# Kernel tuning notes

Measured on AMD Instinct MI355X. Metric: run time of the kernel, lower is better.

## Reference

```python
import jax, jax.numpy as jnp
import numpy as np

WS = 8  # window size
NH = 6  # num heads


def _rel_pos_index(ws):
    coords = jnp.stack(jnp.meshgrid(jnp.arange(ws), jnp.arange(ws), indexing='ij'))  # (2, ws, ws)
    cf = coords.reshape(2, -1)                      # (2, ws*ws)
    rel = cf[:, :, None] - cf[:, None, :]           # (2, ws2, ws2)
    return (rel[0] + ws - 1) * (2 * ws - 1) + (rel[1] + ws - 1)  # (ws2, ws2) int


def setup_inputs() -> dict:
    key = jax.random.key(0)
    k1, k2, k3, k4, k5 = jax.random.split(key, 5)
    B, H, W, C = 4, 256, 256, 192
    dim = C
    x = jax.random.normal(k1, (B, H * W, C), dtype=jnp.float32)
    qkv_w = jax.random.normal(k2, (3 * dim, dim), dtype=jnp.float32) * (dim ** -0.5)
    proj_w = jax.random.normal(k3, (dim, dim), dtype=jnp.float32) * (dim ** -0.5)
    proj_b = jax.random.normal(k4, (dim,), dtype=jnp.float32) * 0.01
    rpb_table = jax.random.normal(k5, ((2 * WS - 1) ** 2, NH), dtype=jnp.float32) * 0.02
    return {"x": x, "qkv_w": qkv_w, "proj_w": proj_w, "proj_b": proj_b,
            "rpb_table": rpb_table, "H": H, "W": W}


def reference(x, qkv_w, proj_w, proj_b, rpb_table, H, W):
    B, L, C = x.shape
    ws, nh = WS, NH
    hd = C // nh
    scale = hd ** -0.5
    ws2 = ws * ws

    pad_r = (ws - W % ws) % ws
    pad_b = (ws - H % ws) % ws
    Hp, Wp = H + pad_b, W + pad_r
    xi = x.reshape(B, H, W, C)
    if pad_r > 0 or pad_b > 0:
        xi = jnp.pad(xi, ((0, 0), (0, pad_b), (0, pad_r), (0, 0)))

    # window partition -> (nW, ws2, C)
    win = xi.reshape(B, Hp // ws, ws, Wp // ws, ws, C)
    win = win.transpose(0, 1, 3, 2, 4, 5).reshape(-1, ws2, C)

    # qkv projection (no bias)
    qkv = (win @ qkv_w.T).reshape(-1, ws2, 3, nh, hd)
    q = qkv[:, :, 0].transpose(0, 2, 1, 3) * scale  # (nW, nh, ws2, hd)
    k = qkv[:, :, 1].transpose(0, 2, 1, 3)
    v = qkv[:, :, 2].transpose(0, 2, 1, 3)

    attn = jnp.einsum('nhqd,nhkd->nhqk', q, k)      # (nW, nh, ws2, ws2)
    bias = rpb_table[_rel_pos_index(ws)]            # (ws2, ws2, nh)
    attn = attn + bias.transpose(2, 0, 1)[None]
    attn = jax.nn.softmax(attn, axis=-1)

    out = jnp.einsum('nhqk,nhkd->nhqd', attn, v)    # (nW, nh, ws2, hd)
    out = out.transpose(0, 2, 1, 3).reshape(-1, ws2, C)
    out = out @ proj_w.T + proj_b

    # window reverse
    xo = out.reshape(B, Hp // ws, Wp // ws, ws, ws, C)
    xo = xo.transpose(0, 1, 3, 2, 4, 5).reshape(B, Hp, Wp, C)
    if pad_r > 0 or pad_b > 0:
        xo = xo[:, :H, :W, :]
    return xo.reshape(B, H * W, C)
```

## Files before the change

kernel.cpp:

```cpp
#include <hip/hip_runtime.h>

typedef _Float16 f16;
typedef _Float16 f16x8 __attribute__((ext_vector_type(8)));
typedef _Float16 f16x4 __attribute__((ext_vector_type(4)));
typedef __fp16 h16x2 __attribute__((ext_vector_type(2)));
typedef float f32x4 __attribute__((ext_vector_type(4)));

constexpr int HDIM = 256, WDIM = 256, C_ = 192, NH_ = 6;
constexpr float SCALE = 0.17677669529663687f;
constexpr float L2E = 1.4426950408889634f;
constexpr float SCALE2 = SCALE * L2E;
constexpr int XP = 200;
constexpr int BUF = 64 * XP;

#define SCHED_FENCE() __builtin_amdgcn_sched_barrier(0)

constexpr size_t OFF_WQ   = 0;
constexpr size_t OFF_WP   = 221184;
constexpr size_t OFF_BIAS = 294912;

__global__ __launch_bounds__(256) void prep_kernel(const float* __restrict__ qkv_w,
                                                   const float* __restrict__ proj_w,
                                                   const float* __restrict__ rpb,
                                                   f16* __restrict__ wqp, f16* __restrict__ wpp,
                                                   float* __restrict__ biasp) {
    int i = blockIdx.x * 256 + threadIdx.x;
    if (i < 13824) {
        int lane = i & 63, rest = i >> 6;
        int ks = rest % 6; rest /= 6;
        int dt = rest & 1; rest >>= 1;
        int c = rest % 3, w = rest / 3;
        int l15 = lane & 15, lg = lane >> 4;
        int row = c * 192 + w * 32 + dt * 16 + l15;
        int col = ks * 32 + lg * 8;
        float sc = (c == 0) ? SCALE2 : 1.0f;
#pragma unroll
        for (int j = 0; j < 8; ++j) wqp[(size_t)i * 8 + j] = (f16)(qkv_w[row * 192 + col + j] * sc);
    } else if (i < 18432) {
        int g = i - 13824;
        int lane = g & 63, rest = g >> 6;
        int ks = rest % 6; rest /= 6;
        int nt = rest & 1, w = rest >> 1;
        int l15 = lane & 15, lg = lane >> 4;
        int row = w * 32 + nt * 16 + l15;
        int col = ks * 32 + lg * 8;
#pragma unroll
        for (int j = 0; j < 8; ++j) wpp[(size_t)g * 8 + j] = (f16)proj_w[row * 192 + col + j];
    } else if (i < 24576) {
        int g = i - 18432;
        int lane = g & 63;
        int kt = (g >> 6) & 3, qt = (g >> 8) & 3, h = g >> 10;
        int q = qt * 16 + (lane & 15);
#pragma unroll
        for (int j = 0; j < 4; ++j) {
            int k = kt * 16 + (lane >> 4) * 4 + j;
            int dy = (q >> 3) - (k >> 3) + 7;
            int dx = (q & 7) - (k & 7) + 7;
            biasp[(size_t)g * 4 + j] = rpb[(dy * 15 + dx) * NH_ + h] * L2E;
        }
    }
}

__global__ __launch_bounds__(256, 3) void fused_kernel(const float* __restrict__ x,
                                                       const f16* __restrict__ wqp,
                                                       const f16* __restrict__ wpp,
                                                       const float* __restrict__ pb,
                                                       const float* __restrict__ biasp,
                                                       float* __restrict__ out) {
    __shared__ f16 xlds[2 * BUF];
    const int tid = threadIdx.x;
    const int v = tid >> 6;
    const int lane = tid & 63;
    const int l15 = lane & 15, lg = lane >> 4;
    const int wb = blockIdx.x * 2;
    const int win = wb + (v >> 1);
    const int b = win >> 10, wy = (win >> 5) & 31, wx = win & 31;
    f16* mylds = xlds + (v >> 1) * BUF;

#pragma unroll
    for (int grp = 0; grp < 3; ++grp) {
#pragma unroll
        for (int it8 = 0; it8 < 8; ++it8) {
            int u = tid + (grp * 8 + it8) * 256;
            int wh = (u >= 3072) ? 1 : 0;
            int r = u - wh * 3072;
            int row = r / 48, c4 = r - row * 48;
            int ws = wb + wh;
            int bs = ws >> 10, wys = (ws >> 5) & 31, wxs = ws & 31;
            int gy = wys * 8 + (row >> 3), gx = wxs * 8 + (row & 7);
            float4 vv = *((const float4*)(x + ((size_t)((bs * HDIM + gy) * WDIM + gx)) * C_ + c4 * 4));
            h16x2 p0 = __builtin_amdgcn_cvt_pkrtz(vv.x, vv.y);
            h16x2 p1 = __builtin_amdgcn_cvt_pkrtz(vv.z, vv.w);
            f16x4 o4;
            o4[0] = (f16)p0[0]; o4[1] = (f16)p0[1]; o4[2] = (f16)p1[0]; o4[3] = (f16)p1[1];
            *((f16x4*)(xlds + wh * BUF + row * XP + c4 * 4)) = o4;
        }
        SCHED_FENCE();
    }
    __syncthreads();

    f16x4 oreg[3][4][2];

#pragma unroll
    for (int hh = 0; hh < 3; ++hh) {
        const int head = (v & 1) * 3 + hh;
        const f16x8* wqb   = (const f16x8*)wqp + (size_t)head * 36 * 64 + lane;
        const f32x4* bbase = (const f32x4*)biasp + (size_t)head * 16 * 64 + lane;
        SCHED_FENCE();

        f16x4 qf[2][4], kf[2][4];
        {
            f32x4 aq[2][4], ak[2][4];
#pragma unroll
            for (int ii = 0; ii < 4; ++ii)
#pragma unroll
                for (int jj = 0; jj < 2; ++jj) {
                    f32x4 z = {0.f, 0.f, 0.f, 0.f};
                    aq[jj][ii] = z; ak[jj][ii] = z;
                }
            __builtin_amdgcn_s_setprio(1);
#pragma unroll
            for (int ks = 0; ks < 6; ++ks) {
                f16x8 Wq0 = wqb[(size_t)(     ks) * 64], Wq1 = wqb[(size_t)( 6 + ks) * 64];
                f16x8 Wk0 = wqb[(size_t)(12 + ks) * 64], Wk1 = wqb[(size_t)(18 + ks) * 64];
#pragma unroll
                for (int tt = 0; tt < 4; ++tt) {
                    f16x8 xt = *((const f16x8*)(mylds + (tt * 16 + l15) * XP + ks * 32 + lg * 8));
                    aq[0][tt] = __builtin_amdgcn_mfma_f32_16x16x32_f16(Wq0, xt, aq[0][tt], 0, 0, 0);
                    aq[1][tt] = __builtin_amdgcn_mfma_f32_16x16x32_f16(Wq1, xt, aq[1][tt], 0, 0, 0);
                    ak[0][tt] = __builtin_amdgcn_mfma_f32_16x16x32_f16(Wk0, xt, ak[0][tt], 0, 0, 0);
                    ak[1][tt] = __builtin_amdgcn_mfma_f32_16x16x32_f16(Wk1, xt, ak[1][tt], 0, 0, 0);
                }
            }
            __builtin_amdgcn_s_setprio(0);
#pragma unroll
            for (int dt = 0; dt < 2; ++dt)
#pragma unroll
                for (int tt = 0; tt < 4; ++tt)
#pragma unroll
                    for (int ii = 0; ii < 4; ++ii) {
                        qf[dt][tt][ii] = (f16)(aq[dt][tt][ii]);
                        kf[dt][tt][ii] = (f16)(ak[dt][tt][ii]);
                    }
        }
        SCHED_FENCE();

        f16x4 vf[4][2];
        {
            f32x4 av[4][2];
#pragma unroll
            for (int ii = 0; ii < 4; ++ii)
#pragma unroll
                for (int jj = 0; jj < 2; ++jj) { f32x4 z = {0.f,0.f,0.f,0.f}; av[ii][jj] = z; }
            __builtin_amdgcn_s_setprio(1);
#pragma unroll
            for (int ks = 0; ks < 6; ++ks) {
                f16x8 W0 = wqb[(size_t)(24 + ks) * 64], W1 = wqb[(size_t)(30 + ks) * 64];
#pragma unroll
                for (int tt = 0; tt < 4; ++tt) {
                    f16x8 xt = *((const f16x8*)(mylds + (tt * 16 + l15) * XP + ks * 32 + lg * 8));
                    av[tt][0] = __builtin_amdgcn_mfma_f32_16x16x32_f16(xt, W0, av[tt][0], 0, 0, 0);
                    av[tt][1] = __builtin_amdgcn_mfma_f32_16x16x32_f16(xt, W1, av[tt][1], 0, 0, 0);
                }
            }
            __builtin_amdgcn_s_setprio(0);
#pragma unroll
            for (int tt = 0; tt < 4; ++tt)
#pragma unroll
                for (int dt = 0; dt < 2; ++dt)
#pragma unroll
                    for (int ii = 0; ii < 4; ++ii)
                        vf[tt][dt][ii] = (f16)(av[tt][dt][ii]);
        }
        SCHED_FENCE();

#pragma unroll
        for (int qt = 0; qt < 4; ++qt) {
            f32x4 s[4];
#pragma unroll
            for (int kt = 0; kt < 4; ++kt) {
                f32x4 bb = bbase[(size_t)(qt * 4 + kt) * 64];
                s[kt] = __builtin_amdgcn_mfma_f32_16x16x16f16(kf[0][kt], qf[0][qt], bb, 0, 0, 0);
                s[kt] = __builtin_amdgcn_mfma_f32_16x16x16f16(kf[1][kt], qf[1][qt], s[kt], 0, 0, 0);
            }
            float m = s[0][0];
#pragma unroll
            for (int kt = 0; kt < 4; ++kt)
#pragma unroll
                for (int ii = 0; ii < 4; ++ii) m = fmaxf(m, s[kt][ii]);
            m = fmaxf(m, __shfl_xor(m, 16));
            m = fmaxf(m, __shfl_xor(m, 32));
            float sum = 0.f;
            f16x4 pa[4];
#pragma unroll
            for (int kt = 0; kt < 4; ++kt)
#pragma unroll
                for (int ii = 0; ii < 4; ++ii) {
                    float e;
                    asm("v_exp_f32 %0, %1" : "=v"(e) : "v"(s[kt][ii] - m));
                    sum += e;
                    pa[kt][ii] = (f16)e;
                }
            sum += __shfl_xor(sum, 16);
            sum += __shfl_xor(sum, 32);
            const float rq = __builtin_amdgcn_rcpf(sum);

#pragma unroll
            for (int dt = 0; dt < 2; ++dt) {
                f32x4 z = {0.f, 0.f, 0.f, 0.f};
                f32x4 o0 = __builtin_amdgcn_mfma_f32_16x16x16f16(vf[0][dt], pa[0], z, 0, 0, 0);
                o0 = __builtin_amdgcn_mfma_f32_16x16x16f16(vf[1][dt], pa[1], o0, 0, 0, 0);
                f32x4 o1 = __builtin_amdgcn_mfma_f32_16x16x16f16(vf[2][dt], pa[2], z, 0, 0, 0);
                o1 = __builtin_amdgcn_mfma_f32_16x16x16f16(vf[3][dt], pa[3], o1, 0, 0, 0);
                f32x4 o = o0 + o1;
                f16x4 ov;
#pragma unroll
                for (int ii = 0; ii < 4; ++ii) ov[ii] = (f16)(o[ii] * rq);
                oreg[hh][qt][dt] = ov;
            }
        }
    }
    SCHED_FENCE();
    __syncthreads();

#pragma unroll
    for (int hh = 0; hh < 3; ++hh) {
        const int head = (v & 1) * 3 + hh;
#pragma unroll
        for (int qt = 0; qt < 4; ++qt)
#pragma unroll
            for (int dt = 0; dt < 2; ++dt)
                *((f16x4*)(mylds + (qt * 16 + l15) * XP + head * 32 + dt * 16 + lg * 4)) = oreg[hh][qt][dt];
    }
    SCHED_FENCE();
    __syncthreads();

#pragma unroll
    for (int hh = 0; hh < 3; ++hh) {
        const int head = (v & 1) * 3 + hh;
        const f16x8* wpb = (const f16x8*)wpp + (size_t)head * 12 * 64 + lane;
#pragma unroll
        for (int nt = 0; nt < 2; ++nt) {
            f16x8 wpf[6];
#pragma unroll
            for (int ks = 0; ks < 6; ++ks)
                wpf[ks] = wpb[(size_t)(nt * 6 + ks) * 64];
            f32x4 bv = *((const f32x4*)(pb + head * 32 + nt * 16 + lg * 4));
#pragma unroll
            for (int qt = 0; qt < 4; ++qt) {
                f32x4 acc = {0.f, 0.f, 0.f, 0.f};
#pragma unroll
                for (int ks = 0; ks < 6; ++ks) {
                    f16x8 af = *((const f16x8*)(mylds + (qt * 16 + l15) * XP + ks * 32 + lg * 8));
                    acc = __builtin_amdgcn_mfma_f32_16x16x32_f16(wpf[ks], af, acc, 0, 0, 0);
                }
                acc += bv;
                const int t = qt * 16 + l15;
                const int gy = wy * 8 + (t >> 3), gx = wx * 8 + (t & 7);
                *((f32x4*)(out + ((size_t)((b * HDIM + gy) * WDIM + gx)) * C_ + head * 32 + nt * 16 + lg * 4)) = acc;
            }
        }
    }
}

extern "C" void kernel_launch(void* const* d_in, const int* in_sizes, int n_in,
                              void* d_out, int out_size, void* d_ws, size_t ws_size,
                              hipStream_t stream) {
    const float* x      = (const float*)d_in[0];
    const float* qkv_w  = (const float*)d_in[1];
    const float* proj_w = (const float*)d_in[2];
    const float* proj_b = (const float*)d_in[3];
    const float* rpb    = (const float*)d_in[4];
    float* out = (float*)d_out;
    char* ws = (char*)d_ws;
    f16* wqp     = (f16*)(ws + OFF_WQ);
    f16* wpp     = (f16*)(ws + OFF_WP);
    float* biasp = (float*)(ws + OFF_BIAS);

    prep_kernel<<<96, 256, 0, stream>>>(qkv_w, proj_w, rpb, wqp, wpp, biasp);
    fused_kernel<<<2048, 256, 0, stream>>>(x, wqp, wpp, proj_b, biasp, out);
}
```

Before: 174.6 us.

## Use tiled fragment-major LDS layout for window activations and restructure proj loop

Replaces the padded row-major LDS tile (row stride 200) with a tiled layout where each 16-row by 32-column MFMA fragment sits in a contiguous 512-element block. Each lane's f16x8 operand then lands at a linear offset. The global load now reads 8 floats per thread and writes an f16x8 to LDS, and the attention-output store uses the same tiled layout. The projection loop is reordered to load the A-fragments once per q-tile and reuse them across both output column tiles, and an asm KEEP pins the output registers. This aims to cut LDS bank conflicts and redundant LDS reads, at the cost of more live registers under the occupancy-3 launch bound.

```diff
diff --git a/kernel.cpp b/kernel.cpp
--- a/kernel.cpp
+++ b/kernel.cpp
@@ -10,10 +10,10 @@
 constexpr float SCALE = 0.17677669529663687f;
 constexpr float L2E = 1.4426950408889634f;
 constexpr float SCALE2 = SCALE * L2E;
-constexpr int XP = 200;
-constexpr int BUF = 64 * XP;
+constexpr int BUF = 12288;
 
 #define SCHED_FENCE() __builtin_amdgcn_sched_barrier(0)
+#define KEEP(v) asm volatile("" : "+v"(v))
 
 constexpr size_t OFF_WQ   = 0;
 constexpr size_t OFF_WP   = 221184;
@@ -76,26 +76,29 @@
     const int win = wb + (v >> 1);
     const int b = win >> 10, wy = (win >> 5) & 31, wx = win & 31;
     f16* mylds = xlds + (v >> 1) * BUF;
-
-#pragma unroll
-    for (int grp = 0; grp < 3; ++grp) {
-#pragma unroll
-        for (int it8 = 0; it8 < 8; ++it8) {
-            int u = tid + (grp * 8 + it8) * 256;
-            int wh = (u >= 3072) ? 1 : 0;
-            int r = u - wh * 3072;
-            int row = r / 48, c4 = r - row * 48;
-            int ws = wb + wh;
-            int bs = ws >> 10, wys = (ws >> 5) & 31, wxs = ws & 31;
-            int gy = wys * 8 + (row >> 3), gx = wxs * 8 + (row & 7);
-            float4 vv = *((const float4*)(x + ((size_t)((bs * HDIM + gy) * WDIM + gx)) * C_ + c4 * 4));
-            h16x2 p0 = __builtin_amdgcn_cvt_pkrtz(vv.x, vv.y);
-            h16x2 p1 = __builtin_amdgcn_cvt_pkrtz(vv.z, vv.w);
-            f16x4 o4;
-            o4[0] = (f16)p0[0]; o4[1] = (f16)p0[1]; o4[2] = (f16)p1[0]; o4[3] = (f16)p1[1];
-            *((f16x4*)(xlds + wh * BUF + row * XP + c4 * 4)) = o4;
-        }
-        SCHED_FENCE();
+    const int lbase = lg * 128 + l15 * 8;
+    const int obase = (lg >> 1) * 128 + l15 * 8 + (lg & 1) * 4;
+
+#pragma unroll
+    for (int it = 0; it < 12; ++it) {
+        int u = tid + it * 256;
+        int wh = (u >= 1536) ? 1 : 0;
+        int r = u - wh * 1536;
+        int row = r & 63, cg = r >> 6;
+        int ws = wb + wh;
+        int bs = ws >> 10, wys = (ws >> 5) & 31, wxs = ws & 31;
+        int gy = wys * 8 + (row >> 3), gx = wxs * 8 + (row & 7);
+        const float4* sp = (const float4*)(x + ((size_t)((bs * HDIM + gy) * WDIM + gx)) * C_ + cg * 8);
+        float4 u0 = sp[0], u1 = sp[1];
+        h16x2 p0 = __builtin_amdgcn_cvt_pkrtz(u0.x, u0.y);
+        h16x2 p1 = __builtin_amdgcn_cvt_pkrtz(u0.z, u0.w);
+        h16x2 p2 = __builtin_amdgcn_cvt_pkrtz(u1.x, u1.y);
+        h16x2 p3 = __builtin_amdgcn_cvt_pkrtz(u1.z, u1.w);
+        f16x8 o8;
+        o8[0] = (f16)p0[0]; o8[1] = (f16)p0[1]; o8[2] = (f16)p1[0]; o8[3] = (f16)p1[1];
+        o8[4] = (f16)p2[0]; o8[5] = (f16)p2[1]; o8[6] = (f16)p3[0]; o8[7] = (f16)p3[1];
+        *((f16x8*)(xlds + wh * BUF + (((row >> 4) * 24 + cg) << 7) + ((row & 15) << 3))) = o8;
+        if ((it & 3) == 3) SCHED_FENCE();
     }
     __syncthreads();
 
@@ -125,7 +128,7 @@
                 f16x8 Wk0 = wqb[(size_t)(12 + ks) * 64], Wk1 = wqb[(size_t)(18 + ks) * 64];
 #pragma unroll
                 for (int tt = 0; tt < 4; ++tt) {
-                    f16x8 xt = *((const f16x8*)(mylds + (tt * 16 + l15) * XP + ks * 32 + lg * 8));
+                    f16x8 xt = *((const f16x8*)(mylds + ((tt * 6 + ks) << 9) + lbase));
                     aq[0][tt] = __builtin_amdgcn_mfma_f32_16x16x32_f16(Wq0, xt, aq[0][tt], 0, 0, 0);
                     aq[1][tt] = __builtin_amdgcn_mfma_f32_16x16x32_f16(Wq1, xt, aq[1][tt], 0, 0, 0);
                     ak[0][tt] = __builtin_amdgcn_mfma_f32_16x16x32_f16(Wk0, xt, ak[0][tt], 0, 0, 0);
@@ -158,7 +161,7 @@
                 f16x8 W0 = wqb[(size_t)(24 + ks) * 64], W1 = wqb[(size_t)(30 + ks) * 64];
 #pragma unroll
                 for (int tt = 0; tt < 4; ++tt) {
-                    f16x8 xt = *((const f16x8*)(mylds + (tt * 16 + l15) * XP + ks * 32 + lg * 8));
+                    f16x8 xt = *((const f16x8*)(mylds + ((tt * 6 + ks) << 9) + lbase));
                     av[tt][0] = __builtin_amdgcn_mfma_f32_16x16x32_f16(xt, W0, av[tt][0], 0, 0, 0);
                     av[tt][1] = __builtin_amdgcn_mfma_f32_16x16x32_f16(xt, W1, av[tt][1], 0, 0, 0);
                 }
@@ -217,6 +220,7 @@
 #pragma unroll
                 for (int ii = 0; ii < 4; ++ii) ov[ii] = (f16)(o[ii] * rq);
                 oreg[hh][qt][dt] = ov;
+                KEEP(oreg[hh][qt][dt]);
             }
         }
     }
@@ -230,7 +234,7 @@
         for (int qt = 0; qt < 4; ++qt)
 #pragma unroll
             for (int dt = 0; dt < 2; ++dt)
-                *((f16x4*)(mylds + (qt * 16 + l15) * XP + head * 32 + dt * 16 + lg * 4)) = oreg[hh][qt][dt];
+                *((f16x4*)(mylds + ((qt * 6 + head) << 9) + dt * 256 + obase)) = oreg[hh][qt][dt];
     }
     SCHED_FENCE();
     __syncthreads();
@@ -239,25 +243,33 @@
     for (int hh = 0; hh < 3; ++hh) {
         const int head = (v & 1) * 3 + hh;
         const f16x8* wpb = (const f16x8*)wpp + (size_t)head * 12 * 64 + lane;
-#pragma unroll
-        for (int nt = 0; nt < 2; ++nt) {
-            f16x8 wpf[6];
+        f16x8 wpf[2][6];
+#pragma unroll
+        for (int nt = 0; nt < 2; ++nt)
 #pragma unroll
             for (int ks = 0; ks < 6; ++ks)
-                wpf[ks] = wpb[(size_t)(nt * 6 + ks) * 64];
-            f32x4 bv = *((const f32x4*)(pb + head * 32 + nt * 16 + lg * 4));
-#pragma unroll
-            for (int qt = 0; qt < 4; ++qt) {
+                wpf[nt][ks] = wpb[(size_t)(nt * 6 + ks) * 64];
+        f32x4 bv[2];
+#pragma unroll
+        for (int nt = 0; nt < 2; ++nt)
+            bv[nt] = *((const f32x4*)(pb + head * 32 + nt * 16 + lg * 4));
+#pragma unroll
+        for (int qt = 0; qt < 4; ++qt) {
+            f16x8 af[6];
+#pragma unroll
+            for (int ks = 0; ks < 6; ++ks)
+                af[ks] = *((const f16x8*)(mylds + ((qt * 6 + ks) << 9) + lbase));
+            const int t = qt * 16 + l15;
+            const int gy = wy * 8 + (t >> 3), gx = wx * 8 + (t & 7);
+            float* orow = out + ((size_t)((b * HDIM + gy) * WDIM + gx)) * C_ + head * 32;
+#pragma unroll
+            for (int nt = 0; nt < 2; ++nt) {
                 f32x4 acc = {0.f, 0.f, 0.f, 0.f};
 #pragma unroll
-                for (int ks = 0; ks < 6; ++ks) {
-                    f16x8 af = *((const f16x8*)(mylds + (qt * 16 + l15) * XP + ks * 32 + lg * 8));
-                    acc = __builtin_amdgcn_mfma_f32_16x16x32_f16(wpf[ks], af, acc, 0, 0, 0);
-                }
-                acc += bv;
-                const int t = qt * 16 + l15;
-                const int gy = wy * 8 + (t >> 3), gx = wx * 8 + (t & 7);
-                *((f32x4*)(out + ((size_t)((b * HDIM + gy) * WDIM + gx)) * C_ + head * 32 + nt * 16 + lg * 4)) = acc;
+                for (int ks = 0; ks < 6; ++ks)
+                    acc = __builtin_amdgcn_mfma_f32_16x16x32_f16(wpf[nt][ks], af[ks], acc, 0, 0, 0);
+                acc += bv[nt];
+                *((f32x4*)(orow + nt * 16 + lg * 4)) = acc;
             }
         }
     }
```

New measurement: 167.3 us. 4.2% less time.
